# Kernel tuning notes

Measured on AMD Instinct MI355X. Metric: run time of the kernel, lower is better.

Reference implementation:

```python
import jax, jax.numpy as jnp
import numpy as np
import math

C = 256
GROUPS = 8
EPS = 1e-5

def setup_inputs() -> dict:
    key = jax.random.key(0)
    ks = jax.random.split(key, 10)
    b, c, h, w = 4, C, 64, 64
    x = jax.random.normal(ks[0], (b, c, h, w), dtype=jnp.float32)
    scale = 1.0 / math.sqrt(c)
    wq = jax.random.normal(ks[1], (c, c), dtype=jnp.float32) * scale
    wk = jax.random.normal(ks[2], (c, c), dtype=jnp.float32) * scale
    wv = jax.random.normal(ks[3], (c, c), dtype=jnp.float32) * scale
    wp = jax.random.normal(ks[4], (c, c), dtype=jnp.float32) * scale
    bq = jnp.zeros((c,), jnp.float32)
    bk = jnp.zeros((c,), jnp.float32)
    bv = jnp.zeros((c,), jnp.float32)
    bp = jnp.zeros((c,), jnp.float32)
    gamma = jnp.ones((c,), jnp.float32)
    beta = jnp.zeros((c,), jnp.float32)
    return {"x": x, "gamma": gamma, "beta": beta, "wq": wq, "bq": bq,
            "wk": wk, "bk": bk, "wv": wv, "bv": bv, "wp": wp, "bp": bp}

def _group_norm(x, gamma, beta):
    b, c, h, w = x.shape
    xr = x.reshape(b, GROUPS, c // GROUPS, h, w)
    mean = xr.mean(axis=(2, 3, 4), keepdims=True)
    var = xr.var(axis=(2, 3, 4), keepdims=True)
    xn = ((xr - mean) * jax.lax.rsqrt(var + EPS)).reshape(b, c, h, w)
    return xn * gamma[None, :, None, None] + beta[None, :, None, None]

def _conv1x1(x, w, bias):
    # 1x1 conv == channel matmul: [b,c,h,w] x [out,in] -> [b,out,h,w]
    return jnp.einsum('bchw,dc->bdhw', x, w) + bias[None, :, None, None]

def reference(x, gamma, beta, wq, bq, wk, bk, wv, bv, wp, bp):
    b, c, h, w = x.shape
    residual = x
    xn = _group_norm(x, gamma, beta)
    q = _conv1x1(xn, wq, bq).reshape(b, c, h * w).transpose(0, 2, 1)  # [b, hw, c]
    k = _conv1x1(xn, wk, bk).reshape(b, c, h * w)                    # [b, c, hw]
    v = _conv1x1(xn, wv, bv).reshape(b, c, h * w).transpose(0, 2, 1)  # [b, hw, c]
    attn = jnp.einsum('bqc,bck->bqk', q, k) / jnp.sqrt(jnp.float32(c))
    attn = jax.nn.softmax(attn, axis=-1)
    out = jnp.einsum('bqk,bkc->bqc', attn, v)                         # [b, hw, c]
    out = out.transpose(0, 2, 1).reshape(b, c, h, w)
    out = _conv1x1(out, wp, bp)
    return out + residual
```

## Files before the change

### kernel.cpp

```cpp
#include <hip/hip_runtime.h>

#define HW 4096
#define CD 256
#define KB 32
#define NKB 64
#define NSP 2
#define C1 0.09016844f

typedef __bf16 bf16x8v __attribute__((ext_vector_type(8)));
typedef float f32x4 __attribute__((ext_vector_type(4)));
typedef unsigned short u16;
typedef unsigned int u32;
typedef u16 u16x4 __attribute__((ext_vector_type(4)));
typedef u16 u16x8 __attribute__((ext_vector_type(8)));

static __device__ __forceinline__ u16 f2bf(float f){
  __bf16 h = (__bf16)f;
  return __builtin_bit_cast(u16, h);
}
static __device__ __forceinline__ float bf2f(u16 v){
  u32 u = ((u32)v) << 16;
  return __builtin_bit_cast(float, u);
}

static __device__ __forceinline__ f32x4 MFMA(u16x8 a, u16x8 b, f32x4 c){
  return __builtin_amdgcn_mfma_f32_16x16x32_bf16(
      __builtin_bit_cast(bf16x8v, a), __builtin_bit_cast(bf16x8v, b), c, 0, 0, 0);
}

#define GLL16(gsrc, ldst) __builtin_amdgcn_global_load_lds( \
    (const __attribute__((address_space(1))) void*)(gsrc),  \
    (__attribute__((address_space(3))) void*)(ldst), 16, 0, 0)

__global__ void k_gn1(const float* __restrict__ x,
                      const float* __restrict__ wq, const float* __restrict__ wk,
                      const float* __restrict__ wv, const float* __restrict__ wp,
                      u16* __restrict__ Wbf, float* __restrict__ gpart){
  int g = blockIdx.x, b = blockIdx.y, ck = blockIdx.z;
  int tid = threadIdx.x;
  {
    int bid = (ck*4 + b)*8 + g;
    int i4 = bid*1024 + tid*4;
    int z = i4 >> 16, off = i4 & 65535;
    const float* src = (z==0)?wq:(z==1)?wk:(z==2)?wv:wp;
    float4 v = *(const float4*)(src + off);
    u16x4 o = { f2bf(v.x), f2bf(v.y), f2bf(v.z), f2bf(v.w) };
    *(u16x4*)(Wbf + i4) = o;
  }
  const float* xp = x + ((size_t)(b*CD) + g*32)*HW + ck*512;
  float s0 = 0.f, s1 = 0.f;
  #pragma unroll
  for (int j = 0; j < 16; ++j){
    int idx = j*1024 + tid*4;
    float4 v = *(const float4*)(xp + (size_t)(idx >> 9)*HW + (idx & 511));
    s0 += v.x + v.y + v.z + v.w;
    s1 += v.x*v.x + v.y*v.y + v.z*v.z + v.w*v.w;
  }
  #pragma unroll
  for (int m = 1; m < 64; m <<= 1){ s0 += __shfl_xor(s0, m); s1 += __shfl_xor(s1, m); }
  __shared__ float red[8];
  int lane = tid & 63, wave = tid >> 6;
  if (lane == 0){ red[wave] = s0; red[4+wave] = s1; }
  __syncthreads();
  if (tid == 0){
    float* dst = gpart + ((b*8 + g)*8 + ck)*2;
    dst[0] = red[0]+red[1]+red[2]+red[3];
    dst[1] = red[4]+red[5]+red[6]+red[7];
  }
}

__global__ void k_gn2(const float* __restrict__ x, const float* __restrict__ gamma,
                      const float* __restrict__ beta, const float* __restrict__ gpart,
                      u16* __restrict__ xnT){
  int g = blockIdx.x, b = blockIdx.y, ck = blockIdx.z;
  int tid = threadIdx.x;
  float s0 = 0.f, s1 = 0.f;
  #pragma unroll
  for (int s = 0; s < 8; ++s){
    const float* p = gpart + ((b*8 + g)*8 + s)*2;
    s0 += p[0]; s1 += p[1];
  }
  float inv_n = 1.0f/(32.0f*HW);
  float mean = s0*inv_n;
  float var = s1*inv_n - mean*mean;
  float rstd = rsqrtf(var + 1e-5f);
  int pl = tid >> 2, c8 = (tid & 3)*8;
  float av[8], bv_[8];
  #pragma unroll
  for (int e = 0; e < 8; ++e){
    int c = g*32 + c8 + e;
    float a = rstd * gamma[c];
    av[e] = a;
    bv_[e] = beta[c] - mean*a;
  }
  const float* xb = x + (size_t)(b*CD + g*32 + c8)*HW;
  #pragma unroll
  for (int it = 0; it < 8; ++it){
    int p = ck*512 + it*64 + pl;
    u16x8 o;
    #pragma unroll
    for (int e = 0; e < 8; ++e){
      float v = xb[(size_t)e*HW + p];
      o[e] = f2bf(v*av[e] + bv_[e]);
    }
    *(u16x8*)(xnT + ((size_t)(b*HW) + p)*CD + g*32 + c8) = o;
  }
}

__global__ __launch_bounds__(256,2) void k_qkv(const u16* __restrict__ xnT, const u16* __restrict__ Wbf,
    const float* __restrict__ bq, const float* __restrict__ bk, const float* __restrict__ bv,
    u16* __restrict__ Q, u16* __restrict__ K, u16* __restrict__ V){
  __shared__ u16 tile[4][4096];
  int z = blockIdx.z, b = blockIdx.y, pbase = blockIdx.x*64;
  int tid = threadIdx.x, lane = tid & 63, wave = tid >> 6;
  int lq = lane & 15, lg = lane >> 4;
  const u16* W = Wbf + z*65536;
  const float* bias = (z==0)?bq:(z==1)?bk:bv;
  float scl = (z==0) ? C1 : 1.0f;
  int nbase = wave*64;
  f32x4 acc[4][4] = {};
  #pragma unroll
  for (int kk = 0; kk < 8; ++kk){
    u16x8 af[4], bf[4];
    #pragma unroll
    for (int m = 0; m < 4; ++m)
      af[m] = *(const u16x8*)(xnT + ((size_t)(b*HW + pbase + m*16 + lq))*CD + kk*32 + lg*8);
    #pragma unroll
    for (int n = 0; n < 4; ++n)
      bf[n] = *(const u16x8*)(W + (size_t)(nbase + n*16 + lq)*CD + kk*32 + lg*8);
    #pragma unroll
    for (int m = 0; m < 4; ++m)
      #pragma unroll
      for (int n = 0; n < 4; ++n)
        acc[m][n] = MFMA(af[m], bf[n], acc[m][n]);
  }
  #pragma unroll
  for (int n = 0; n < 4; ++n){
    float bb = bias[nbase + n*16 + lq];
    #pragma unroll
    for (int m = 0; m < 4; ++m)
      #pragma unroll
      for (int r = 0; r < 4; ++r)
        acc[m][n][r] = (acc[m][n][r] + bb) * scl;
  }
  if (z == 2){
    #pragma unroll
    for (int m = 0; m < 4; ++m)
      #pragma unroll
      for (int n = 0; n < 4; ++n){
        int d = nbase + n*16 + lq;
        int p0 = pbase + m*16 + lg*4;
        u16x4 o = { f2bf(acc[m][n][0]), f2bf(acc[m][n][1]), f2bf(acc[m][n][2]), f2bf(acc[m][n][3]) };
        *(u16x4*)(V + (size_t)(b*CD + d)*HW + p0) = o;
      }
  } else {
    u16* dst = (z==0)?Q:K;
    u16* tl = tile[wave];
    #pragma unroll
    for (int m = 0; m < 4; ++m)
      #pragma unroll
      for (int n = 0; n < 4; ++n)
        #pragma unroll
        for (int r = 0; r < 4; ++r){
          int row = m*16 + lg*4 + r;
          int col = n*16 + lq;
          tl[row*64 + ((((col>>3) + row) & 7)<<3) + (col & 7)] = f2bf(acc[m][n][r]);
        }
    #pragma unroll
    for (int j = 0; j < 8; ++j){
      int idx = j*64 + lane;
      int row = idx >> 3, ch = idx & 7;
      u16x8 v = *(const u16x8*)(tl + row*64 + (((ch + row)&7)<<3));
      *(u16x8*)(dst + ((size_t)(b*HW + pbase + row))*CD + nbase + ch*8) = v;
    }
  }
}

__global__ __launch_bounds__(512,4) void k_attn(const u16* __restrict__ Q, const u16* __restrict__ K,
    const u16* __restrict__ V, u16* __restrict__ Opart, float2* __restrict__ ml){
  extern __shared__ char smem[];
  int tid = threadIdx.x, lane = tid & 63, wave = tid >> 6;
  int lq = lane & 15, lg = lane >> 4;
  int pair = wave >> 1, half = wave & 1;
  int qt = blockIdx.x, sp = blockIdx.y, b = blockIdx.z;
  int qbase = qt*64 + pair*16;
  int key0 = sp*(NKB*KB);

  int ke[2], ve[2];
  #pragma unroll
  for (int i = 0; i < 2; ++i){
    int G = i*512 + tid;
    int kr = G >> 5;
    ke[i] = kr*CD + (((G & 31) ^ kr) & 31)*8;
    int vrow = G >> 3;
    int p = (G >> 2) & 1;
    int j = ((G & 3) - vrow) & 3;
    ve[i] = (vrow*2 + p)*HW + j*8;
  }
  int bvo = (lq>>1)*128 + (((lq&1)*4 + ((lg + (lq>>1)) & 3)))*16;

  u16x8 qa[8];
  #pragma unroll
  for (int cc = 0; cc < 8; ++cc)
    qa[cc] = *(const u16x8*)(Q + ((size_t)(b*HW + qbase + lq))*CD + cc*32 + lg*8);

  f32x4 o[8] = {};
  float m_ = 0.f, l_ = 0.f;

  const u16* Kb = K + (size_t)(b*HW + key0)*CD;
  const u16* Vb = V + (size_t)(b*CD)*HW + key0;
  char* Pw = smem + 65536 + pair*1024;
  float* mb = (float*)(smem + 69632);

  {
    char* kd = smem; char* vd = smem + 32768;
    #pragma unroll
    for (int i = 0; i < 2; ++i){
      GLL16(Kb + ke[i], kd + i*8192 + wave*1024);
      GLL16(Vb + ve[i], vd + i*8192 + wave*1024);
    }
  }
  __syncthreads();
  int cur = 0;
  for (int kb = 0; kb < NKB; ++kb){
    if (kb + 1 < NKB){
      char* kd = smem + (cur^1)*16384;
      const u16* kg = Kb + (size_t)(kb+1)*KB*CD;
      #pragma unroll
      for (int i = 0; i < 2; ++i)
        GLL16(kg + ke[i], kd + i*8192 + wave*1024);
    }
    const char* kt = smem + cur*16384;

    f32x4 sa = (f32x4){0.f,0.f,0.f,0.f};
    int row = half*16 + lq;
    #pragma unroll
    for (int cc = 0; cc < 8; ++cc){
      int ch = cc*4 + lg;
      u16x8 kf = *(const u16x8*)(kt + row*512 + (((ch ^ row) & 31) << 4));
      sa = MFMA(kf, qa[cc], sa);
    }
    float v = fmaxf(fmaxf(sa[0], sa[1]), fmaxf(sa[2], sa[3]));
    v = fmaxf(v, __shfl_xor(v, 16));
    v = fmaxf(v, __shfl_xor(v, 32));
    if (lg == 0) mb[pair*32 + half*16 + lq] = v;
    float rs;
    {
      float p0 = exp2f(sa[0] - m_), p1 = exp2f(sa[1] - m_);
      float p2 = exp2f(sa[2] - m_), p3 = exp2f(sa[3] - m_);
      rs = (p0 + p1) + (p2 + p3);
      u32 w0 = (u32)f2bf(p0) | ((u32)f2bf(p1) << 16);
      u32 w1 = (u32)f2bf(p2) | ((u32)f2bf(p3) << 16);
      int chunk = 2*half + (lg>>1);
      int slot  = (chunk + (lq>>1)) & 3;
      int base  = (lq>>1)*128 + ((lq&1)*4 + slot)*16;
      *(u32*)(Pw + base + ((2*lg + 0)&3)*4) = w0;
      *(u32*)(Pw + base + ((2*lg + 1)&3)*4) = w1;
    }
    rs += __shfl_xor(rs, 16);
    rs += __shfl_xor(rs, 32);
    l_ += rs;
    if (kb + 1 < NKB)
      asm volatile("s_waitcnt vmcnt(2) lgkmcnt(0)" ::: "memory");
    else
      asm volatile("s_waitcnt vmcnt(0) lgkmcnt(0)" ::: "memory");
    __builtin_amdgcn_s_barrier();
    __builtin_amdgcn_sched_barrier(0);

    if (kb + 1 < NKB){
      char* vd = smem + 32768 + (cur^1)*16384;
      const u16* vg = Vb + (kb+1)*KB;
      #pragma unroll
      for (int i = 0; i < 2; ++i)
        GLL16(vg + ve[i], vd + i*8192 + wave*1024);
    }
    float mx = fmaxf(mb[pair*32 + lq], mb[pair*32 + 16 + lq]);
    u16x8 pa = *(const u16x8*)(Pw + bvo);
    const char* vt = smem + 32768 + cur*16384;
    #pragma unroll
    for (int f = 0; f < 8; ++f){
      u16x8 vf = *(const u16x8*)(vt + (half*8 + f)*1024 + bvo);
      o[f] = MFMA(pa, vf, o[f]);
    }
    if (!__all(mx <= m_ + 8.0f)){
      float nm = fmaxf(m_, mx);
      float corr = exp2f(m_ - nm);
      m_ = nm;
      l_ *= corr;
      float cr[4];
      #pragma unroll
      for (int r = 0; r < 4; ++r)
        cr[r] = __shfl(corr, lg*4 + r);
      #pragma unroll
      for (int f = 0; f < 8; ++f)
        #pragma unroll
        for (int r = 0; r < 4; ++r)
          o[f][r] *= cr[r];
    }
    if (kb + 1 < NKB){
      asm volatile("s_waitcnt vmcnt(2)" ::: "memory");
      __builtin_amdgcn_s_barrier();
      __builtin_amdgcn_sched_barrier(0);
    }
    cur ^= 1;
  }
  __syncthreads();
  if (lg == 0) mb[pair*32 + half*16 + lq] = l_;
  __syncthreads();
  float l_tot = mb[pair*32 + lq] + mb[pair*32 + 16 + lq];
  size_t ob = ((size_t)((sp*4 + b)*HW + qbase))*CD;
  #pragma unroll
  for (int f = 0; f < 8; ++f){
    int c = (half*8 + f)*16 + lq;
    #pragma unroll
    for (int r = 0; r < 4; ++r)
      Opart[ob + (size_t)(lg*4 + r)*CD + c] = f2bf(o[f][r]);
  }
  if (half == 0 && lg == 0)
    ml[(size_t)(sp*4 + b)*HW + qbase + lq] = make_float2(m_, l_tot);
}

__global__ void k_comb(const u16* __restrict__ Opart, const float2* __restrict__ ml,
                       u16* __restrict__ Opm){
  int b = blockIdx.y;
  int q = blockIdx.x*8 + (threadIdx.x >> 5);
  int c0 = (threadIdx.x & 31)*8;
  float2 e[NSP];
  float m = -3.0e38f;
  #pragma unroll
  for (int s = 0; s < NSP; ++s){
    e[s] = ml[(size_t)(s*4 + b)*HW + q];
    m = fmaxf(m, e[s].x);
  }
  float w[NSP], den = 0.f;
  #pragma unroll
  for (int s = 0; s < NSP; ++s){
    w[s] = exp2f(e[s].x - m);
    den += e[s].y * w[s];
  }
  float inv = 1.0f / den;
  float sum[8] = {};
  #pragma unroll
  for (int s = 0; s < NSP; ++s){
    u16x8 v = *(const u16x8*)(Opart + ((size_t)((s*4 + b)*HW) + q)*CD + c0);
    float ws = w[s];
    #pragma unroll
    for (int t = 0; t < 8; ++t)
      sum[t] += bf2f(v[t]) * ws;
  }
  u16x8 o;
  #pragma unroll
  for (int t = 0; t < 8; ++t)
    o[t] = f2bf(sum[t]*inv);
  *(u16x8*)(Opm + ((size_t)(b*HW) + q)*CD + c0) = o;
}

__global__ __launch_bounds__(256,2) void k_proj(const u16* __restrict__ Opm, const u16* __restrict__ Wp,
    const float* __restrict__ bp, const float* __restrict__ x, float* __restrict__ out){
  int b = blockIdx.y, pbase = blockIdx.x*32;
  int tid = threadIdx.x, lane = tid & 63, wave = tid >> 6;
  int lq = lane & 15, lg = lane >> 4;
  int nbase = wave*64;
  f32x4 acc[2][4] = {};
  #pragma unroll
  for (int kk = 0; kk < 8; ++kk){
    u16x8 af[2], bf[4];
    #pragma unroll
    for (int m = 0; m < 2; ++m)
      af[m] = *(const u16x8*)(Opm + ((size_t)(b*HW + pbase + m*16 + lq))*CD + kk*32 + lg*8);
    #pragma unroll
    for (int n = 0; n < 4; ++n)
      bf[n] = *(const u16x8*)(Wp + (size_t)(nbase + n*16 + lq)*CD + kk*32 + lg*8);
    #pragma unroll
    for (int m = 0; m < 2; ++m)
      #pragma unroll
      for (int n = 0; n < 4; ++n)
        acc[m][n] = MFMA(af[m], bf[n], acc[m][n]);
  }
  #pragma unroll
  for (int m = 0; m < 2; ++m)
    #pragma unroll
    for (int n = 0; n < 4; ++n){
      int d = nbase + n*16 + lq;
      int p0 = pbase + m*16 + lg*4;
      size_t base = (size_t)(b*CD + d)*HW + p0;
      float bb = bp[d];
      float4 res = *(const float4*)(x + base);
      float4 ov;
      ov.x = acc[m][n][0] + bb + res.x;
      ov.y = acc[m][n][1] + bb + res.y;
      ov.z = acc[m][n][2] + bb + res.z;
      ov.w = acc[m][n][3] + bb + res.w;
      *(float4*)(out + base) = ov;
    }
}

extern "C" void kernel_launch(void* const* d_in, const int* in_sizes, int n_in,
                              void* d_out, int out_size, void* d_ws, size_t ws_size,
                              hipStream_t stream){
  const float* x     = (const float*)d_in[0];
  const float* gamma = (const float*)d_in[1];
  const float* beta  = (const float*)d_in[2];
  const float* wq    = (const float*)d_in[3];
  const float* bq    = (const float*)d_in[4];
  const float* wk    = (const float*)d_in[5];
  const float* bk    = (const float*)d_in[6];
  const float* wv    = (const float*)d_in[7];
  const float* bv    = (const float*)d_in[8];
  const float* wp    = (const float*)d_in[9];
  const float* bp    = (const float*)d_in[10];
  float* out = (float*)d_out;

  char* ws = (char*)d_ws;
  u16*   xnT   = (u16*)(ws);
  u16*   Qb    = (u16*)(ws + (8ull<<20));
  u16*   Kb    = (u16*)(ws + (16ull<<20));
  u16*   Vb    = (u16*)(ws + (24ull<<20));
  u16*   Opm   = (u16*)(ws + (32ull<<20));
  u16*   Wbf   = (u16*)(ws + (40ull<<20));
  float2* mlb  = (float2*)(ws + (40ull<<20) + (512ull<<10));
  u16*   Opart = (u16*)(ws + (41ull<<20));
  float* gpart = (float*)Qb;

  hipFuncSetAttribute((const void*)k_attn, hipFuncAttributeMaxDynamicSharedMemorySize, 70144);

  k_gn1 <<<dim3(8,4,8), 256, 0, stream>>>(x, wq, wk, wv, wp, Wbf, gpart);
  k_gn2 <<<dim3(8,4,8), 256, 0, stream>>>(x, gamma, beta, gpart, xnT);
  k_qkv <<<dim3(64,4,3), 256, 0, stream>>>(xnT, Wbf, bq, bk, bv, Qb, Kb, Vb);
  k_attn<<<dim3(64,NSP,4), 512, 70144, stream>>>(Qb, Kb, Vb, Opart, mlb);
  k_comb<<<dim3(512,4), 256, 0, stream>>>(Opart, mlb, Opm);
  k_proj<<<dim3(128,4), 256, 0, stream>>>(Opm, Wbf + 3*65536, bp, x, out);
}
```

Measured before the change: 163.0 us.

## Fuse split-KV combine into projection and stage bf16 copy of x for groupnorm

The separate combine kernel is removed. The projection GEMM now reads both split-KV partial outputs, computes the log-sum-exp weights per row, and blends the partials while loading its A operand. Separately, the first groupnorm pass writes a bf16 copy of x so the second pass reads half the bytes. This saves one launch and an intermediate round trip, but the projection does redundant blend work per wave, normalization now starts from bf16-rounded inputs, and the extra bf16 write in gn1 adds traffic.

New measurement: 161.8 us. No clear change (-0.7%).

```diff
diff --git a/kernel.cpp b/kernel.cpp
--- a/kernel.cpp
+++ b/kernel.cpp
@@ -35,7 +35,8 @@
 __global__ void k_gn1(const float* __restrict__ x,
                       const float* __restrict__ wq, const float* __restrict__ wk,
                       const float* __restrict__ wv, const float* __restrict__ wp,
-                      u16* __restrict__ Wbf, float* __restrict__ gpart){
+                      u16* __restrict__ Wbf, u16* __restrict__ xb16,
+                      float* __restrict__ gpart){
   int g = blockIdx.x, b = blockIdx.y, ck = blockIdx.z;
   int tid = threadIdx.x;
   {
@@ -47,14 +48,19 @@
     u16x4 o = { f2bf(v.x), f2bf(v.y), f2bf(v.z), f2bf(v.w) };
     *(u16x4*)(Wbf + i4) = o;
   }
-  const float* xp = x + ((size_t)(b*CD) + g*32)*HW + ck*512;
+  size_t xoff = ((size_t)(b*CD) + g*32)*HW + ck*512;
+  const float* xp = x + xoff;
+  u16* xbp = xb16 + xoff;
   float s0 = 0.f, s1 = 0.f;
   #pragma unroll
   for (int j = 0; j < 16; ++j){
     int idx = j*1024 + tid*4;
-    float4 v = *(const float4*)(xp + (size_t)(idx >> 9)*HW + (idx & 511));
+    size_t eo = (size_t)(idx >> 9)*HW + (idx & 511);
+    float4 v = *(const float4*)(xp + eo);
     s0 += v.x + v.y + v.z + v.w;
     s1 += v.x*v.x + v.y*v.y + v.z*v.z + v.w*v.w;
+    u16x4 o = { f2bf(v.x), f2bf(v.y), f2bf(v.z), f2bf(v.w) };
+    *(u16x4*)(xbp + eo) = o;
   }
   #pragma unroll
   for (int m = 1; m < 64; m <<= 1){ s0 += __shfl_xor(s0, m); s1 += __shfl_xor(s1, m); }
@@ -69,7 +75,7 @@
   }
 }
 
-__global__ void k_gn2(const float* __restrict__ x, const float* __restrict__ gamma,
+__global__ void k_gn2(const u16* __restrict__ xb16, const float* __restrict__ gamma,
                       const float* __restrict__ beta, const float* __restrict__ gpart,
                       u16* __restrict__ xnT){
   int g = blockIdx.x, b = blockIdx.y, ck = blockIdx.z;
@@ -93,14 +99,14 @@
     av[e] = a;
     bv_[e] = beta[c] - mean*a;
   }
-  const float* xb = x + (size_t)(b*CD + g*32 + c8)*HW;
+  const u16* xb = xb16 + (size_t)(b*CD + g*32 + c8)*HW;
   #pragma unroll
   for (int it = 0; it < 8; ++it){
     int p = ck*512 + it*64 + pl;
     u16x8 o;
     #pragma unroll
     for (int e = 0; e < 8; ++e){
-      float v = xb[(size_t)e*HW + p];
+      float v = bf2f(xb[(size_t)e*HW + p]);
       o[e] = f2bf(v*av[e] + bv_[e]);
     }
     *(u16x8*)(xnT + ((size_t)(b*HW) + p)*CD + g*32 + c8) = o;
@@ -320,54 +326,37 @@
     ml[(size_t)(sp*4 + b)*HW + qbase + lq] = make_float2(m_, l_tot);
 }
 
-__global__ void k_comb(const u16* __restrict__ Opart, const float2* __restrict__ ml,
-                       u16* __restrict__ Opm){
-  int b = blockIdx.y;
-  int q = blockIdx.x*8 + (threadIdx.x >> 5);
-  int c0 = (threadIdx.x & 31)*8;
-  float2 e[NSP];
-  float m = -3.0e38f;
-  #pragma unroll
-  for (int s = 0; s < NSP; ++s){
-    e[s] = ml[(size_t)(s*4 + b)*HW + q];
-    m = fmaxf(m, e[s].x);
-  }
-  float w[NSP], den = 0.f;
-  #pragma unroll
-  for (int s = 0; s < NSP; ++s){
-    w[s] = exp2f(e[s].x - m);
-    den += e[s].y * w[s];
-  }
-  float inv = 1.0f / den;
-  float sum[8] = {};
-  #pragma unroll
-  for (int s = 0; s < NSP; ++s){
-    u16x8 v = *(const u16x8*)(Opart + ((size_t)((s*4 + b)*HW) + q)*CD + c0);
-    float ws = w[s];
-    #pragma unroll
-    for (int t = 0; t < 8; ++t)
-      sum[t] += bf2f(v[t]) * ws;
-  }
-  u16x8 o;
-  #pragma unroll
-  for (int t = 0; t < 8; ++t)
-    o[t] = f2bf(sum[t]*inv);
-  *(u16x8*)(Opm + ((size_t)(b*HW) + q)*CD + c0) = o;
-}
-
-__global__ __launch_bounds__(256,2) void k_proj(const u16* __restrict__ Opm, const u16* __restrict__ Wp,
+__global__ __launch_bounds__(256,2) void k_proj(const u16* __restrict__ Opart,
+    const float2* __restrict__ ml, const u16* __restrict__ Wp,
     const float* __restrict__ bp, const float* __restrict__ x, float* __restrict__ out){
   int b = blockIdx.y, pbase = blockIdx.x*32;
   int tid = threadIdx.x, lane = tid & 63, wave = tid >> 6;
   int lq = lane & 15, lg = lane >> 4;
   int nbase = wave*64;
+  float w0[2], w1[2];
+  #pragma unroll
+  for (int m = 0; m < 2; ++m){
+    int p = pbase + m*16 + lq;
+    float2 e0 = ml[(size_t)(b)*HW + p];
+    float2 e1 = ml[(size_t)(4 + b)*HW + p];
+    float mm = fmaxf(e0.x, e1.x);
+    float q0 = exp2f(e0.x - mm), q1 = exp2f(e1.x - mm);
+    float inv = 1.0f / (e0.y*q0 + e1.y*q1);
+    w0[m] = q0*inv; w1[m] = q1*inv;
+  }
   f32x4 acc[2][4] = {};
   #pragma unroll
   for (int kk = 0; kk < 8; ++kk){
     u16x8 af[2], bf[4];
     #pragma unroll
-    for (int m = 0; m < 2; ++m)
-      af[m] = *(const u16x8*)(Opm + ((size_t)(b*HW + pbase + m*16 + lq))*CD + kk*32 + lg*8);
+    for (int m = 0; m < 2; ++m){
+      int p = pbase + m*16 + lq;
+      u16x8 a0 = *(const u16x8*)(Opart + ((size_t)(b*HW + p))*CD + kk*32 + lg*8);
+      u16x8 a1 = *(const u16x8*)(Opart + ((size_t)((4 + b)*HW + p))*CD + kk*32 + lg*8);
+      #pragma unroll
+      for (int t = 0; t < 8; ++t)
+        af[m][t] = f2bf(bf2f(a0[t])*w0[m] + bf2f(a1[t])*w1[m]);
+    }
     #pragma unroll
     for (int n = 0; n < 4; ++n)
       bf[n] = *(const u16x8*)(Wp + (size_t)(nbase + n*16 + lq)*CD + kk*32 + lg*8);
@@ -416,7 +405,7 @@
   u16*   Qb    = (u16*)(ws + (8ull<<20));
   u16*   Kb    = (u16*)(ws + (16ull<<20));
   u16*   Vb    = (u16*)(ws + (24ull<<20));
-  u16*   Opm   = (u16*)(ws + (32ull<<20));
+  u16*   xb16  = (u16*)(ws + (32ull<<20));
   u16*   Wbf   = (u16*)(ws + (40ull<<20));
   float2* mlb  = (float2*)(ws + (40ull<<20) + (512ull<<10));
   u16*   Opart = (u16*)(ws + (41ull<<20));
@@ -424,10 +413,9 @@
 
   hipFuncSetAttribute((const void*)k_attn, hipFuncAttributeMaxDynamicSharedMemorySize, 70144);
 
-  k_gn1 <<<dim3(8,4,8), 256, 0, stream>>>(x, wq, wk, wv, wp, Wbf, gpart);
-  k_gn2 <<<dim3(8,4,8), 256, 0, stream>>>(x, gamma, beta, gpart, xnT);
+  k_gn1 <<<dim3(8,4,8), 256, 0, stream>>>(x, wq, wk, wv, wp, Wbf, xb16, gpart);
+  k_gn2 <<<dim3(8,4,8), 256, 0, stream>>>(xb16, gamma, beta, gpart, xnT);
   k_qkv <<<dim3(64,4,3), 256, 0, stream>>>(xnT, Wbf, bq, bk, bv, Qb, Kb, Vb);
   k_attn<<<dim3(64,NSP,4), 512, 70144, stream>>>(Qb, Kb, Vb, Opart, mlb);
-  k_comb<<<dim3(512,4), 256, 0, stream>>>(Opart, mlb, Opm);
-  k_proj<<<dim3(128,4), 256, 0, stream>>>(Opm, Wbf + 3*65536, bp, x, out);
-}
+  k_proj<<<dim3(128,4), 256, 0, stream>>>(Opart, mlb, Wbf + 3*65536, bp, x, out);
+}
```
